# Performance work log

Hardware: AMD Instinct MI355X
Metric: run time of the kernel (lower is better)

## Reference

```python
import jax, jax.numpy as jnp
import numpy as np

APPERTURE = 256
LN_EPS = 1e-3  # keras LayerNormalization default


def _layernorm(x, gamma, beta):
    mu = jnp.mean(x, axis=-1, keepdims=True)
    var = jnp.mean(jnp.square(x - mu), axis=-1, keepdims=True)
    return (x - mu) * jax.lax.rsqrt(var + LN_EPS) * gamma + beta


def setup_inputs() -> dict:
    key = jax.random.key(0)
    ks = jax.random.split(key, 8)
    n, d = 4096, 1024
    s = 0.02
    return {
        "x": jax.random.normal(ks[0], (1, n, d), jnp.float32),
        "wk": s * jax.random.normal(ks[1], (d, d), jnp.float32),
        "wq": s * jax.random.normal(ks[2], (d, d), jnp.float32),
        "wv": s * jax.random.normal(ks[3], (d, d), jnp.float32),
        "wo": s * jax.random.normal(ks[4], (d, d), jnp.float32),
        "wka": s * jax.random.normal(ks[5], (d, d), jnp.float32),
        "bka": jnp.zeros((d,), jnp.float32),
        "wkd": s * jax.random.normal(ks[6], (d, 1), jnp.float32),
        "bkd": jnp.zeros((1,), jnp.float32),
        "g_y": jnp.ones((d,), jnp.float32),
        "b_y": jnp.zeros((d,), jnp.float32),
        "g_ka": jnp.ones((d,), jnp.float32),
        "b_ka": jnp.zeros((d,), jnp.float32),
    }


def reference(x, wk, wq, wv, wo, wka, bka, wkd, bkd, g_y, b_y, g_ka, b_ka):
    m = x.shape[2]
    xf = x.reshape(-1, m)            # (n, m); seqlen == max_seqlen so no pad/trunc
    n = xf.shape[0]
    K = xf @ wk                      # (n, d)
    Q = (xf @ wq) * 0.06             # (n, d)
    V = xf @ wv                      # (n, d)
    logits = Q @ K.T                 # (n, n)
    # banded (apperture) mask: entries with |i-j| > apperture -> -inf
    idx = jnp.arange(n)
    band = jnp.abs(idx[:, None] - idx[None, :]) <= APPERTURE
    logits = jnp.where(band, logits, -jnp.inf)
    weights = jax.nn.softmax(logits, axis=0)   # softmax over queries (axis 0), as in original
    # y = transpose(V^T @ W) = W^T @ V
    y = weights.T @ V                # (n, d)
    y = y @ wo + xf                  # output_linear (no bias) + residual
    y = _layernorm(y, g_y, b_y)
    y = jax.nn.relu(y @ wka + bka)
    y = _layernorm(y, g_ka, b_ka)
    y = jax.nn.sigmoid(y @ wkd + bkd)  # (n, 1)
    return y.reshape(1, -1)            # (1, n)
```

## Files before the change

### kernel.cpp

```cpp
#include <hip/hip_runtime.h>
#include <hip/hip_bf16.h>
#include <math.h>

typedef __hip_bfloat16 bf16;
typedef __attribute__((ext_vector_type(8))) short bf16x8;
typedef __attribute__((ext_vector_type(4))) float f32x4;

#define NROW 4096
#define DIM  1024
#define APP  256
#define WIN  640
#define VTPW 4608
#define OLD  2048

__device__ __forceinline__ unsigned short f2bu(float f) {
    bf16 h = __float2bfloat16(f);
    return *reinterpret_cast<unsigned short*>(&h);
}
__device__ __forceinline__ float bu2f(unsigned short u) {
    bf16 h; *reinterpret_cast<unsigned short*>(&h) = u;
    return __bfloat162float(h);
}
__device__ __forceinline__ unsigned pk2(float a, float b) {
    return (unsigned)f2bu(a) | ((unsigned)f2bu(b) << 16);
}
__device__ __forceinline__ void gload_lds16(const void* g, void* l) {
    __builtin_amdgcn_global_load_lds(
        (const __attribute__((address_space(1))) unsigned int*)g,
        (__attribute__((address_space(3))) unsigned int*)l, 16, 0, 0);
}

struct PrepArgs { const float* x; bf16* xb; const float* srcw[5]; bf16* dstw[5]; bf16* Vtp; };
__global__ __launch_bounds__(256) void prep_kernel(PrepArgs p) {
    __shared__ float T[64][65];
    const int bid = blockIdx.x, t = threadIdx.x;
    if (bid < 2048) {
        size_t base = ((size_t)bid * 256 + t) * 8;
        float4 v0 = *(const float4*)(p.x + base);
        float4 v1 = *(const float4*)(p.x + base + 4);
        uint4 o;
        o.x = pk2(v0.x, v0.y); o.y = pk2(v0.z, v0.w);
        o.z = pk2(v1.x, v1.y); o.w = pk2(v1.z, v1.w);
        *(uint4*)(p.xb + base) = o;
        return;
    }
    if (bid < 3328) {
        int r = bid - 2048;
        const int z = r >> 8; r &= 255;
        const int r0 = (r & 15) * 64, c0 = (r >> 4) * 64;
        const float* in = p.srcw[z];
        bf16* out = p.dstw[z];
        if (z < 3) {
            #pragma unroll
            for (int c = 0; c < 4; ++c) {
                int row = (t >> 4) + c * 16, col = (t & 15) * 4;
                float4 v = *(const float4*)(in + (size_t)(r0 + row) * 1024 + c0 + col);
                uint2 o; o.x = pk2(v.x, v.y); o.y = pk2(v.z, v.w);
                *(uint2*)(out + (size_t)(r0 + row) * 1024 + c0 + col) = o;
            }
            return;
        }
        #pragma unroll
        for (int c = 0; c < 4; ++c) {
            int row = (t >> 4) + c * 16, col = (t & 15) * 4;
            float4 v = *(const float4*)(in + (size_t)(r0 + row) * 1024 + c0 + col);
            T[row][col] = v.x; T[row][col + 1] = v.y; T[row][col + 2] = v.z; T[row][col + 3] = v.w;
        }
        __syncthreads();
        #pragma unroll
        for (int c = 0; c < 4; ++c) {
            int orow = (t >> 4) + c * 16, ocol = (t & 15) * 4;
            uint2 o;
            o.x = pk2(T[ocol][orow], T[ocol + 1][orow]);
            o.y = pk2(T[ocol + 2][orow], T[ocol + 3][orow]);
            *(uint2*)(out + (size_t)(c0 + orow) * 1024 + r0 + ocol) = o;
        }
        return;
    }
    {
        int idx = (bid - 3328) * 256 + t;
        int row = idx >> 7;
        int c4  = idx & 127;
        int col = (c4 < 64) ? (c4 * 4) : (4352 + (c4 - 64) * 4);
        *(uint2*)(p.Vtp + (size_t)row * VTPW + col) = (uint2){0u, 0u};
    }
}

template <int BM, int BN>
__global__ __launch_bounds__(256) void gemm_bt(
    const bf16* __restrict__ A, int lda, const bf16* __restrict__ Bt, int ldb,
    bf16* __restrict__ C, int ldc, int K,
    float alpha, const float* __restrict__ bias, int relu, int pv)
{
    constexpr int WM = BM / 2, WN = BN / 2, AI = WM / 16, BJ = WN / 16;
    __shared__ bf16 As[BM * 64];
    __shared__ bf16 Bs[BN * 64];
    const int t = threadIdx.x, l = t & 63, w = t >> 6;
    const int wr = w >> 1, wc = w & 1;
    const int jl = l & 15, g = l >> 4;
    const int m0 = blockIdx.y * BM, n0 = blockIdx.x * BN;
    const bf16* Btb = pv ? (Bt + (size_t)(m0 >> 7) * 128) : Bt;

    f32x4 acc[AI][BJ];
    #pragma unroll
    for (int i = 0; i < AI; ++i)
        #pragma unroll
        for (int j = 0; j < BJ; ++j) acc[i][j] = (f32x4){0.f, 0.f, 0.f, 0.f};

    for (int kk = 0; kk < K; kk += 64) {
        __syncthreads();
        #pragma unroll
        for (int c = 0; c < BM / 32; ++c) {
            int q = t + c * 256;
            int row = q >> 3;
            int kel = ((q & 7) ^ (row & 7)) << 3;
            gload_lds16(A + (size_t)(m0 + row) * lda + kk + kel,
                        (char*)As + (c * 256 + w * 64) * 16);
        }
        #pragma unroll
        for (int c = 0; c < BN / 32; ++c) {
            int q = t + c * 256;
            int row = q >> 3;
            int kel = ((q & 7) ^ (row & 7)) << 3;
            gload_lds16(Btb + (size_t)(n0 + row) * ldb + kk + kel,
                        (char*)Bs + (c * 256 + w * 64) * 16);
        }
        __syncthreads();
        #pragma unroll
        for (int ks = 0; ks < 2; ++ks) {
            bf16x8 af[AI], bfr[BJ];
            #pragma unroll
            for (int i = 0; i < AI; ++i) {
                int ra = wr * WM + i * 16 + jl;
                af[i] = *(const bf16x8*)((char*)As + ra * 128 + ((ks * 64 + g * 16) ^ ((ra & 7) << 4)));
            }
            #pragma unroll
            for (int j = 0; j < BJ; ++j) {
                int rb = wc * WN + j * 16 + jl;
                bfr[j] = *(const bf16x8*)((char*)Bs + rb * 128 + ((ks * 64 + g * 16) ^ ((rb & 7) << 4)));
            }
            #pragma unroll
            for (int i = 0; i < AI; ++i)
                #pragma unroll
                for (int j = 0; j < BJ; ++j)
                    acc[i][j] = __builtin_amdgcn_mfma_f32_16x16x32_bf16(af[i], bfr[j], acc[i][j], 0, 0, 0);
        }
    }

    const int g4 = g * 4;
    #pragma unroll
    for (int j = 0; j < BJ; ++j) {
        int col = n0 + wc * WN + j * 16 + jl;
        float bv = bias ? bias[col] : 0.f;
        #pragma unroll
        for (int i = 0; i < AI; ++i) {
            int rowb = m0 + wr * WM + i * 16 + g4;
            #pragma unroll
            for (int r = 0; r < 4; ++r) {
                float vv = alpha * acc[i][j][r] + bv;
                if (relu) vv = fmaxf(vv, 0.f);
                C[(size_t)(rowb + r) * ldc + col] = __float2bfloat16(vv);
            }
        }
    }
}

struct MiniPtrs { const bf16* A[2]; const bf16* Bt[2]; bf16* C[2]; };
__global__ __launch_bounds__(256) void gemm_mini(MiniPtrs p) {
    constexpr int BM = 128, BN = 64, WM = 64, WN = 32, AI = 4, BJ = 2;
    __shared__ bf16 As[BM * 64];
    __shared__ bf16 Bs[BN * 64];
    const bf16* A  = p.A[blockIdx.z];
    const bf16* Bt = p.Bt[blockIdx.z];
    bf16* C        = p.C[blockIdx.z];
    const int t = threadIdx.x, l = t & 63, w = t >> 6;
    const int wr = w >> 1, wc = w & 1;
    const int jl = l & 15, g = l >> 4;
    const int m0 = blockIdx.y * BM, n0 = blockIdx.x * BN;

    f32x4 acc[AI][BJ];
    #pragma unroll
    for (int i = 0; i < AI; ++i)
        #pragma unroll
        for (int j = 0; j < BJ; ++j) acc[i][j] = (f32x4){0.f, 0.f, 0.f, 0.f};

    for (int kk = 0; kk < DIM; kk += 64) {
        __syncthreads();
        #pragma unroll
        for (int c = 0; c < BM / 32; ++c) {
            int q = t + c * 256;
            int row = q >> 3;
            int kel = ((q & 7) ^ (row & 7)) << 3;
            gload_lds16(A + (size_t)(m0 + row) * DIM + kk + kel,
                        (char*)As + (c * 256 + w * 64) * 16);
        }
        #pragma unroll
        for (int c = 0; c < BN / 32; ++c) {
            int q = t + c * 256;
            int row = q >> 3;
            int kel = ((q & 7) ^ (row & 7)) << 3;
            gload_lds16(Bt + (size_t)(n0 + row) * DIM + kk + kel,
                        (char*)Bs + (c * 256 + w * 64) * 16);
        }
        __syncthreads();
        #pragma unroll
        for (int ks = 0; ks < 2; ++ks) {
            bf16x8 af[AI], bfr[BJ];
            #pragma unroll
            for (int i = 0; i < AI; ++i) {
                int ra = wr * WM + i * 16 + jl;
                af[i] = *(const bf16x8*)((char*)As + ra * 128 + ((ks * 64 + g * 16) ^ ((ra & 7) << 4)));
            }
            #pragma unroll
            for (int j = 0; j < BJ; ++j) {
                int rb = wc * WN + j * 16 + jl;
                bfr[j] = *(const bf16x8*)((char*)Bs + rb * 128 + ((ks * 64 + g * 16) ^ ((rb & 7) << 4)));
            }
            #pragma unroll
            for (int i = 0; i < AI; ++i)
                #pragma unroll
                for (int j = 0; j < BJ; ++j)
                    acc[i][j] = __builtin_amdgcn_mfma_f32_16x16x32_bf16(af[i], bfr[j], acc[i][j], 0, 0, 0);
        }
    }

    const int g4 = g * 4;
    #pragma unroll
    for (int j = 0; j < BJ; ++j) {
        int col = n0 + wc * WN + j * 16 + jl;
        #pragma unroll
        for (int i = 0; i < AI; ++i) {
            int rowb = m0 + wr * WM + i * 16 + g4;
            #pragma unroll
            for (int r = 0; r < 4; ++r)
                C[(size_t)(rowb + r) * DIM + col] = __float2bfloat16(acc[i][j][r]);
        }
    }
}

__global__ __launch_bounds__(256) void tpad_kernel(const bf16* __restrict__ O,
                                                   bf16* __restrict__ Vtp)
{
    __shared__ unsigned short T[64][65];
    const int t = threadIdx.x;
    const int j0 = blockIdx.x * 64, d0 = blockIdx.y * 64;
    #pragma unroll
    for (int c = 0; c < 4; ++c) {
        int row = (t >> 4) + c * 16, col = (t & 15) * 4;
        uint2 v = *(const uint2*)(O + (size_t)(j0 + row) * OLD + 1024 + d0 + col);
        T[row][col]     = (unsigned short)(v.x & 0xffff);
        T[row][col + 1] = (unsigned short)(v.x >> 16);
        T[row][col + 2] = (unsigned short)(v.y & 0xffff);
        T[row][col + 3] = (unsigned short)(v.y >> 16);
    }
    __syncthreads();
    #pragma unroll
    for (int c = 0; c < 4; ++c) {
        int orow = (t >> 4) + c * 16, ocol = (t & 15) * 4;
        uint2 o;
        o.x = (unsigned)T[ocol][orow]     | ((unsigned)T[ocol + 1][orow] << 16);
        o.y = (unsigned)T[ocol + 2][orow] | ((unsigned)T[ocol + 3][orow] << 16);
        *(uint2*)(Vtp + (size_t)(d0 + orow) * VTPW + 256 + j0 + ocol) = o;
    }
}

__global__ __launch_bounds__(256) void score_gemm(const bf16* __restrict__ Qh,
                                                  const bf16* __restrict__ xb,
                                                  bf16* __restrict__ St)
{
    constexpr int WM = 32, WN = 64, AI = 2, BJ = 4;
    __shared__ bf16 As[64 * 64];
    __shared__ bf16 Bs[128 * 64];
    const int t = threadIdx.x, l = t & 63, w = t >> 6;
    const int wr = w >> 1, wc = w & 1;
    const int jl = l & 15, g = l >> 4;
    const int tt = blockIdx.y;
    const int c0 = blockIdx.x * 64;
    const int win0 = tt * 128 - APP;
    const bf16* Kb = xb + (size_t)tt * 128 * DIM;

    f32x4 acc[AI][BJ];
    #pragma unroll
    for (int i = 0; i < AI; ++i)
        #pragma unroll
        for (int j = 0; j < BJ; ++j) acc[i][j] = (f32x4){0.f, 0.f, 0.f, 0.f};

    for (int kk = 0; kk < DIM; kk += 64) {
        __syncthreads();
        #pragma unroll
        for (int c = 0; c < 2; ++c) {
            int q = t + c * 256;
            int row = q >> 3;
            int kel = ((q & 7) ^ (row & 7)) << 3;
            int rg = win0 + c0 + row;
            rg = min(max(rg, 0), NROW - 1);
            gload_lds16(Qh + (size_t)rg * OLD + kk + kel,
                        (char*)As + (c * 256 + w * 64) * 16);
        }
        #pragma unroll
        for (int c = 0; c < 4; ++c) {
            int q = t + c * 256;
            int row = q >> 3;
            int kel = ((q & 7) ^ (row & 7)) << 3;
            gload_lds16(Kb + (size_t)row * DIM + kk + kel,
                        (char*)Bs + (c * 256 + w * 64) * 16);
        }
        __syncthreads();
        #pragma unroll
        for (int ks = 0; ks < 2; ++ks) {
            bf16x8 af[AI], bfr[BJ];
            #pragma unroll
            for (int i = 0; i < AI; ++i) {
                int ra = wr * WM + i * 16 + jl;
                af[i] = *(const bf16x8*)((char*)As + ra * 128 + ((ks * 64 + g * 16) ^ ((ra & 7) << 4)));
            }
            #pragma unroll
            for (int j = 0; j < BJ; ++j) {
                int rb = wc * WN + j * 16 + jl;
                bfr[j] = *(const bf16x8*)((char*)Bs + rb * 128 + ((ks * 64 + g * 16) ^ ((rb & 7) << 4)));
            }
            #pragma unroll
            for (int i = 0; i < AI; ++i)
                #pragma unroll
                for (int j = 0; j < BJ; ++j)
                    acc[i][j] = __builtin_amdgcn_mfma_f32_16x16x32_bf16(af[i], bfr[j], acc[i][j], 0, 0, 0);
        }
    }

    const int g4 = g * 4;
    #pragma unroll
    for (int j = 0; j < BJ; ++j) {
        int coll = wc * WN + j * 16 + jl;
        bf16* strow = St + (size_t)(tt * 128 + coll) * WIN;
        #pragma unroll
        for (int i = 0; i < AI; ++i) {
            int iwb = c0 + wr * WM + i * 16 + g4;
            #pragma unroll
            for (int r = 0; r < 4; ++r)
                strow[iwb + r] = __float2bfloat16(0.06f * acc[i][j][r]);
        }
    }
}

__global__ __launch_bounds__(256) void softmax_band(bf16* __restrict__ St)
{
    const int w = threadIdx.x >> 6, l = threadIdx.x & 63;
    const int j = blockIdx.x * 4 + w;
    const int tt = j >> 7, jt = j & 127;
    unsigned* row = (unsigned*)(St + (size_t)j * WIN);
    const int lo = max(jt, 256 - 128 * tt);
    const int hi = min(jt + 512, 4351 - 128 * tt);
    unsigned u[5]; float v[10];
    #pragma unroll
    for (int c = 0; c < 5; ++c) u[c] = row[l + 64 * c];
    float m = -3e38f;
    #pragma unroll
    for (int c = 0; c < 5; ++c) {
        int iw = 2 * (l + 64 * c);
        v[2 * c]     = (iw >= lo && iw <= hi)         ? bu2f((unsigned short)(u[c] & 0xffff)) : -3e38f;
        v[2 * c + 1] = (iw + 1 >= lo && iw + 1 <= hi) ? bu2f((unsigned short)(u[c] >> 16))    : -3e38f;
        m = fmaxf(m, fmaxf(v[2 * c], v[2 * c + 1]));
    }
    #pragma unroll
    for (int off = 32; off > 0; off >>= 1) m = fmaxf(m, __shfl_xor(m, off));
    float s = 0.f;
    #pragma unroll
    for (int c = 0; c < 10; ++c) {
        float e = (v[c] > -1e37f) ? __expf(v[c] - m) : 0.f;
        v[c] = e; s += e;
    }
    #pragma unroll
    for (int off = 32; off > 0; off >>= 1) s += __shfl_xor(s, off);
    const float inv = 1.f / s;
    #pragma unroll
    for (int c = 0; c < 5; ++c)
        row[l + 64 * c] = pk2(v[2 * c] * inv, v[2 * c + 1] * inv);
}

__global__ __launch_bounds__(256) void ln_kernel(
    const bf16* __restrict__ T, const bf16* __restrict__ Xb,
    const float* __restrict__ g, const float* __restrict__ b, bf16* __restrict__ O)
{
    __shared__ float red1[4], red2[4];
    const int r = blockIdx.x, t = threadIdx.x, lane = t & 63, w = t >> 6;
    ushort4 tv = ((const ushort4*)(T + (size_t)r * DIM))[t];
    float v0 = bu2f(tv.x), v1 = bu2f(tv.y), v2 = bu2f(tv.z), v3 = bu2f(tv.w);
    if (Xb) {
        ushort4 xv = ((const ushort4*)(Xb + (size_t)r * DIM))[t];
        v0 += bu2f(xv.x); v1 += bu2f(xv.y); v2 += bu2f(xv.z); v3 += bu2f(xv.w);
    }
    float s = v0 + v1 + v2 + v3;
    #pragma unroll
    for (int off = 32; off > 0; off >>= 1) s += __shfl_xor(s, off);
    if (lane == 0) red1[w] = s;
    __syncthreads();
    float mu = (red1[0] + red1[1] + red1[2] + red1[3]) * (1.f / DIM);
    float d0 = v0 - mu, d1 = v1 - mu, d2 = v2 - mu, d3 = v3 - mu;
    float s2 = d0 * d0 + d1 * d1 + d2 * d2 + d3 * d3;
    #pragma unroll
    for (int off = 32; off > 0; off >>= 1) s2 += __shfl_xor(s2, off);
    if (lane == 0) red2[w] = s2;
    __syncthreads();
    float var = (red2[0] + red2[1] + red2[2] + red2[3]) * (1.f / DIM);
    float rstd = rsqrtf(var + 1e-3f);
    float4 gv = ((const float4*)g)[t];
    float4 bv = ((const float4*)b)[t];
    uint2 o;
    o.x = pk2(d0 * rstd * gv.x + bv.x, d1 * rstd * gv.y + bv.y);
    o.y = pk2(d2 * rstd * gv.z + bv.z, d3 * rstd * gv.w + bv.w);
    ((uint2*)(O + (size_t)r * DIM))[t] = o;
}

__global__ __launch_bounds__(256) void lnfinal_kernel(
    const bf16* __restrict__ T, const float* __restrict__ g, const float* __restrict__ b,
    const float* __restrict__ wkd, const float* __restrict__ bkd, float* __restrict__ out)
{
    __shared__ float red1[4], red2[4], red3[4];
    const int r = blockIdx.x, t = threadIdx.x, lane = t & 63, w = t >> 6;
    ushort4 tv = ((const ushort4*)(T + (size_t)r * DIM))[t];
    float v0 = bu2f(tv.x), v1 = bu2f(tv.y), v2 = bu2f(tv.z), v3 = bu2f(tv.w);
    float s = v0 + v1 + v2 + v3;
    #pragma unroll
    for (int off = 32; off > 0; off >>= 1) s += __shfl_xor(s, off);
    if (lane == 0) red1[w] = s;
    __syncthreads();
    float mu = (red1[0] + red1[1] + red1[2] + red1[3]) * (1.f / DIM);
    float d0 = v0 - mu, d1 = v1 - mu, d2 = v2 - mu, d3 = v3 - mu;
    float s2 = d0 * d0 + d1 * d1 + d2 * d2 + d3 * d3;
    #pragma unroll
    for (int off = 32; off > 0; off >>= 1) s2 += __shfl_xor(s2, off);
    if (lane == 0) red2[w] = s2;
    __syncthreads();
    float var = (red2[0] + red2[1] + red2[2] + red2[3]) * (1.f / DIM);
    float rstd = rsqrtf(var + 1e-3f);
    float4 gv = ((const float4*)g)[t];
    float4 bv = ((const float4*)b)[t];
    float4 wv = ((const float4*)wkd)[t];
    float s3 = (d0 * rstd * gv.x + bv.x) * wv.x + (d1 * rstd * gv.y + bv.y) * wv.y
             + (d2 * rstd * gv.z + bv.z) * wv.z + (d3 * rstd * gv.w + bv.w) * wv.w;
    #pragma unroll
    for (int off = 32; off > 0; off >>= 1) s3 += __shfl_xor(s3, off);
    if (lane == 0) red3[w] = s3;
    __syncthreads();
    if (t == 0) {
        float tot = red3[0] + red3[1] + red3[2] + red3[3];
        out[r] = 1.f / (1.f + __expf(-(tot + bkd[0])));
    }
}

extern "C" void kernel_launch(void* const* d_in, const int* in_sizes, int n_in,
                              void* d_out, int out_size, void* d_ws, size_t ws_size,
                              hipStream_t stream) {
    const float* x    = (const float*)d_in[0];
    const float* wk   = (const float*)d_in[1];
    const float* wq   = (const float*)d_in[2];
    const float* wv   = (const float*)d_in[3];
    const float* wo   = (const float*)d_in[4];
    const float* wka  = (const float*)d_in[5];
    const float* bka  = (const float*)d_in[6];
    const float* wkd  = (const float*)d_in[7];
    const float* bkd  = (const float*)d_in[8];
    const float* g_y  = (const float*)d_in[9];
    const float* b_y  = (const float*)d_in[10];
    const float* g_ka = (const float*)d_in[11];
    const float* b_ka = (const float*)d_in[12];
    float* out = (float*)d_out;

    char* ws = (char*)d_ws;
    const size_t MB = 1u << 20;
    bf16* wkB  = (bf16*)(ws);
    bf16* wqB  = (bf16*)(ws + 2 * MB);
    bf16* wvB  = (bf16*)(ws + 4 * MB);
    bf16* woT  = (bf16*)(ws + 6 * MB);
    bf16* wkaT = (bf16*)(ws + 8 * MB);
    bf16* WqkT = (bf16*)(ws + 10 * MB);
    bf16* wvoT = (bf16*)(ws + 12 * MB);
    bf16* xb   = (bf16*)(ws + 14 * MB);
    bf16* Obuf = (bf16*)(ws + 22 * MB);
    bf16* Vtp  = (bf16*)(ws + 38 * MB);
    bf16* St   = (bf16*)(ws + 47 * MB);
    bf16* fT   = (bf16*)(ws + 53 * MB);
    bf16* fL1  = (bf16*)(ws + 61 * MB);
    bf16* fRel = (bf16*)(ws + 69 * MB);

    PrepArgs pa;
    pa.x = x; pa.xb = xb; pa.Vtp = Vtp;
    pa.srcw[0] = wk;  pa.srcw[1] = wq;  pa.srcw[2] = wv;  pa.srcw[3] = wo;  pa.srcw[4] = wka;
    pa.dstw[0] = wkB; pa.dstw[1] = wqB; pa.dstw[2] = wvB; pa.dstw[3] = woT; pa.dstw[4] = wkaT;
    prep_kernel<<<3840, 256, 0, stream>>>(pa);

    MiniPtrs mp;
    mp.A[0] = wkB; mp.Bt[0] = wqB; mp.C[0] = WqkT;
    mp.A[1] = woT; mp.Bt[1] = wvB; mp.C[1] = wvoT;
    gemm_mini<<<dim3(16, 8, 2), 256, 0, stream>>>(mp);

    gemm_bt<128, 128><<<dim3(16, 32), 256, 0, stream>>>(
        xb, DIM, WqkT, DIM, Obuf, OLD, DIM, 1.f, nullptr, 0, 0);
    tpad_kernel<<<dim3(64, 16), 256, 0, stream>>>(Obuf, Vtp);

    score_gemm<<<dim3(WIN / 64, NROW / 128), 256, 0, stream>>>(Obuf, xb, St);
    softmax_band<<<NROW / 4, 256, 0, stream>>>(St);
    gemm_bt<64, 128><<<dim3(8, 64), 256, 0, stream>>>(
        St, WIN, Vtp, VTPW, fT, DIM, WIN, 1.f, nullptr, 0, 1);

    ln_kernel<<<NROW, 256, 0, stream>>>(fT, xb, g_y, b_y, fL1);
    gemm_bt<128, 64><<<dim3(16, 32), 256, 0, stream>>>(
        fL1, DIM, wkaT, DIM, fRel, DIM, DIM, 1.f, bka, 1, 0);
    lnfinal_kernel<<<NROW, 256, 0, stream>>>(fRel, g_ka, b_ka, wkd, bkd, out);
}
```

Baseline: 123.2 us.

## Fuse transpose-pad into the projection GEMM epilogue and enlarge GEMM tiles

A dedicated gemm_kqv kernel computes the combined projection and writes the first half straight to a compact Q buffer and the second half transposed into the padded V buffer. This removes the separate tpad_kernel launch and its round trip through a 2048-wide intermediate. The transposed epilogue writes 4-element strided chunks, which are less coalesced than before. The later GEMMs also move to 128x128 tiles, which halves their block counts and may lower occupancy.

After: 129.0 us. +4.7%, slower.

```diff
diff --git a/kernel.cpp b/kernel.cpp
--- a/kernel.cpp
+++ b/kernel.cpp
@@ -11,7 +11,6 @@
 #define APP  256
 #define WIN  640
 #define VTPW 4608
-#define OLD  2048
 
 __device__ __forceinline__ unsigned short f2bu(float f) {
     bf16 h = __float2bfloat16(f);
@@ -165,6 +164,87 @@
     }
 }
 
+__global__ __launch_bounds__(256) void gemm_kqv(
+    const bf16* __restrict__ xb, const bf16* __restrict__ Wcat,
+    bf16* __restrict__ Qh, bf16* __restrict__ Vtp)
+{
+    constexpr int BM = 128, BN = 128, WM = 64, WN = 64, AI = 4, BJ = 4;
+    __shared__ bf16 As[BM * 64];
+    __shared__ bf16 Bs[BN * 64];
+    const int t = threadIdx.x, l = t & 63, w = t >> 6;
+    const int wr = w >> 1, wc = w & 1;
+    const int jl = l & 15, g = l >> 4;
+    const int m0 = blockIdx.y * BM, n0 = blockIdx.x * BN;
+
+    f32x4 acc[AI][BJ];
+    #pragma unroll
+    for (int i = 0; i < AI; ++i)
+        #pragma unroll
+        for (int j = 0; j < BJ; ++j) acc[i][j] = (f32x4){0.f, 0.f, 0.f, 0.f};
+
+    for (int kk = 0; kk < DIM; kk += 64) {
+        __syncthreads();
+        #pragma unroll
+        for (int c = 0; c < 4; ++c) {
+            int q = t + c * 256;
+            int row = q >> 3;
+            int kel = ((q & 7) ^ (row & 7)) << 3;
+            gload_lds16(xb + (size_t)(m0 + row) * DIM + kk + kel,
+                        (char*)As + (c * 256 + w * 64) * 16);
+            gload_lds16(Wcat + (size_t)(n0 + row) * DIM + kk + kel,
+                        (char*)Bs + (c * 256 + w * 64) * 16);
+        }
+        __syncthreads();
+        #pragma unroll
+        for (int ks = 0; ks < 2; ++ks) {
+            bf16x8 af[AI], bfr[BJ];
+            #pragma unroll
+            for (int i = 0; i < AI; ++i) {
+                int ra = wr * WM + i * 16 + jl;
+                af[i] = *(const bf16x8*)((char*)As + ra * 128 + ((ks * 64 + g * 16) ^ ((ra & 7) << 4)));
+            }
+            #pragma unroll
+            for (int j = 0; j < BJ; ++j) {
+                int rb = wc * WN + j * 16 + jl;
+                bfr[j] = *(const bf16x8*)((char*)Bs + rb * 128 + ((ks * 64 + g * 16) ^ ((rb & 7) << 4)));
+            }
+            #pragma unroll
+            for (int i = 0; i < AI; ++i)
+                #pragma unroll
+                for (int j = 0; j < BJ; ++j)
+                    acc[i][j] = __builtin_amdgcn_mfma_f32_16x16x32_bf16(af[i], bfr[j], acc[i][j], 0, 0, 0);
+        }
+    }
+
+    const int g4 = g * 4;
+    if (n0 < 1024) {
+        #pragma unroll
+        for (int j = 0; j < BJ; ++j) {
+            int col = n0 + wc * WN + j * 16 + jl;
+            #pragma unroll
+            for (int i = 0; i < AI; ++i) {
+                int rowb = m0 + wr * WM + i * 16 + g4;
+                #pragma unroll
+                for (int r = 0; r < 4; ++r)
+                    Qh[(size_t)(rowb + r) * DIM + col] = __float2bfloat16(acc[i][j][r]);
+            }
+        }
+    } else {
+        #pragma unroll
+        for (int j = 0; j < BJ; ++j) {
+            int d = n0 - 1024 + wc * WN + j * 16 + jl;
+            #pragma unroll
+            for (int i = 0; i < AI; ++i) {
+                int rowb = m0 + wr * WM + i * 16 + g4;
+                uint2 o;
+                o.x = pk2(acc[i][j][0], acc[i][j][1]);
+                o.y = pk2(acc[i][j][2], acc[i][j][3]);
+                *(uint2*)(Vtp + (size_t)d * VTPW + 256 + rowb) = o;
+            }
+        }
+    }
+}
+
 struct MiniPtrs { const bf16* A[2]; const bf16* Bt[2]; bf16* C[2]; };
 __global__ __launch_bounds__(256) void gemm_mini(MiniPtrs p) {
     constexpr int BM = 128, BN = 64, WM = 64, WN = 32, AI = 4, BJ = 2;
@@ -235,32 +315,6 @@
             for (int r = 0; r < 4; ++r)
                 C[(size_t)(rowb + r) * DIM + col] = __float2bfloat16(acc[i][j][r]);
         }
-    }
-}
-
-__global__ __launch_bounds__(256) void tpad_kernel(const bf16* __restrict__ O,
-                                                   bf16* __restrict__ Vtp)
-{
-    __shared__ unsigned short T[64][65];
-    const int t = threadIdx.x;
-    const int j0 = blockIdx.x * 64, d0 = blockIdx.y * 64;
-    #pragma unroll
-    for (int c = 0; c < 4; ++c) {
-        int row = (t >> 4) + c * 16, col = (t & 15) * 4;
-        uint2 v = *(const uint2*)(O + (size_t)(j0 + row) * OLD + 1024 + d0 + col);
-        T[row][col]     = (unsigned short)(v.x & 0xffff);
-        T[row][col + 1] = (unsigned short)(v.x >> 16);
-        T[row][col + 2] = (unsigned short)(v.y & 0xffff);
-        T[row][col + 3] = (unsigned short)(v.y >> 16);
-    }
-    __syncthreads();
-    #pragma unroll
-    for (int c = 0; c < 4; ++c) {
-        int orow = (t >> 4) + c * 16, ocol = (t & 15) * 4;
-        uint2 o;
-        o.x = (unsigned)T[ocol][orow]     | ((unsigned)T[ocol + 1][orow] << 16);
-        o.y = (unsigned)T[ocol + 2][orow] | ((unsigned)T[ocol + 3][orow] << 16);
-        *(uint2*)(Vtp + (size_t)(d0 + orow) * VTPW + 256 + j0 + ocol) = o;
     }
 }
 
@@ -294,7 +348,7 @@
             int kel = ((q & 7) ^ (row & 7)) << 3;
             int rg = win0 + c0 + row;
             rg = min(max(rg, 0), NROW - 1);
-            gload_lds16(Qh + (size_t)rg * OLD + kk + kel,
+            gload_lds16(Qh + (size_t)rg * DIM + kk + kel,
                         (char*)As + (c * 256 + w * 64) * 16);
         }
         #pragma unroll
@@ -476,12 +530,12 @@
     bf16* WqkT = (bf16*)(ws + 10 * MB);
     bf16* wvoT = (bf16*)(ws + 12 * MB);
     bf16* xb   = (bf16*)(ws + 14 * MB);
-    bf16* Obuf = (bf16*)(ws + 22 * MB);
-    bf16* Vtp  = (bf16*)(ws + 38 * MB);
-    bf16* St   = (bf16*)(ws + 47 * MB);
-    bf16* fT   = (bf16*)(ws + 53 * MB);
-    bf16* fL1  = (bf16*)(ws + 61 * MB);
-    bf16* fRel = (bf16*)(ws + 69 * MB);
+    bf16* Qh   = (bf16*)(ws + 22 * MB);
+    bf16* Vtp  = (bf16*)(ws + 30 * MB);
+    bf16* St   = (bf16*)(ws + 40 * MB);
+    bf16* fT   = (bf16*)(ws + 46 * MB);
+    bf16* fL1  = (bf16*)(ws + 54 * MB);
+    bf16* fRel = (bf16*)(ws + 62 * MB);
 
     PrepArgs pa;
     pa.x = x; pa.xb = xb; pa.Vtp = Vtp;
@@ -494,17 +548,15 @@
     mp.A[1] = woT; mp.Bt[1] = wvB; mp.C[1] = wvoT;
     gemm_mini<<<dim3(16, 8, 2), 256, 0, stream>>>(mp);
 
-    gemm_bt<128, 128><<<dim3(16, 32), 256, 0, stream>>>(
-        xb, DIM, WqkT, DIM, Obuf, OLD, DIM, 1.f, nullptr, 0, 0);
-    tpad_kernel<<<dim3(64, 16), 256, 0, stream>>>(Obuf, Vtp);
-
-    score_gemm<<<dim3(WIN / 64, NROW / 128), 256, 0, stream>>>(Obuf, xb, St);
+    gemm_kqv<<<dim3(16, 32), 256, 0, stream>>>(xb, WqkT, Qh, Vtp);
+
+    score_gemm<<<dim3(WIN / 64, NROW / 128), 256, 0, stream>>>(Qh, xb, St);
     softmax_band<<<NROW / 4, 256, 0, stream>>>(St);
-    gemm_bt<64, 128><<<dim3(8, 64), 256, 0, stream>>>(
+    gemm_bt<128, 128><<<dim3(8, 32), 256, 0, stream>>>(
         St, WIN, Vtp, VTPW, fT, DIM, WIN, 1.f, nullptr, 0, 1);
 
     ln_kernel<<<NROW, 256, 0, stream>>>(fT, xb, g_y, b_y, fL1);
-    gemm_bt<128, 64><<<dim3(16, 32), 256, 0, stream>>>(
+    gemm_bt<128, 128><<<dim3(8, 32), 256, 0, stream>>>(
         fL1, DIM, wkaT, DIM, fRel, DIM, DIM, 1.f, bka, 1, 0);
     lnfinal_kernel<<<NROW, 256, 0, stream>>>(fRel, g_ka, b_ka, wkd, bkd, out);
 }
```
